# Optimization experiments

Hardware: AMD Instinct MI355X
Metric: run time of the kernel (lower is better)

Reference implementation:

```python
import jax, jax.numpy as jnp
import numpy as np

MASK_FILL = -1e9  # masked_fill_value (avoids NaNs vs -inf)

def setup_inputs() -> dict:
    key = jax.random.key(0)
    k1, k2, k3 = jax.random.split(key, 3)
    B, L, H, E = 4, 2048, 16, 128
    S, D = L, E
    queries = jax.random.normal(k1, (B, L, H, E), dtype=jnp.float32)
    keys = jax.random.normal(k2, (B, S, H, E), dtype=jnp.float32)
    values = jax.random.normal(k3, (B, S, H, D), dtype=jnp.float32)
    return {"queries": queries, "keys": keys, "values": values}

def reference(queries, keys, values):
    B, L, H, E = queries.shape
    S = keys.shape[1]
    scale = 1.0 / jnp.sqrt(jnp.asarray(E, queries.dtype))
    # compute_scores: dot-product scores (B,H,L,S)
    scores = jnp.einsum('blhe,bshe->bhls', queries, keys)
    # causal mask (mask_flag=True, attn_mask=None -> TriangularCausalMask)
    causal = jnp.triu(jnp.ones((L, S), dtype=bool), k=1)  # True above diagonal = masked
    scores = jnp.where(causal[None, None, :, :], MASK_FILL, scores)
    # scale * scores -> softmax (dropout p=0, eval)
    A = jax.nn.softmax(scale * scores, axis=-1)
    # combine_values: (B,H,L,S) x (B,S,H,D) -> (B,L,H,D)
    V = jnp.einsum('bhls,bshd->blhd', A, values)
    return V
```

## Files before the change

kernel.cpp:

```cpp
#include <hip/hip_runtime.h>
#include <hip/hip_bf16.h>

typedef __attribute__((ext_vector_type(4))) float f32x4;
typedef __attribute__((ext_vector_type(2))) float f32x2v;
typedef __attribute__((ext_vector_type(16))) float f32x16;
typedef __attribute__((ext_vector_type(8))) short s16x8;
typedef __attribute__((ext_vector_type(4))) short s16x4;
typedef __attribute__((ext_vector_type(4))) unsigned u32x4v;
typedef __attribute__((ext_vector_type(2))) int i32x2;

static constexpr int Bb = 4, Ll = 2048, Hh = 16, Ee = 128;
static constexpr int RS = Hh * Ee;
static constexpr float SCALE = 0.088388347648318447f;
static constexpr float LOG2E = 1.4426950408889634f;
static constexpr float SCL = SCALE * LOG2E;
static constexpr float MOFF = 26.0f;

__device__ __forceinline__ unsigned pk2bf(float lo, float hi) {
  float2 t = make_float2(lo, hi);
  __hip_bfloat162 b2 = __float22bfloat162_rn(t);
  union { __hip_bfloat162 b; unsigned u; } cv; cv.b = b2;
  return cv.u;
}

__device__ __forceinline__ s16x8 pack8(float a0, float a1, float a2, float a3,
                                       float a4, float a5, float a6, float a7) {
  u32x4v u = { pk2bf(a0,a1), pk2bf(a2,a3), pk2bf(a4,a5), pk2bf(a6,a7) };
  return *(s16x8*)&u;
}

__device__ __forceinline__ void plswap(int &x, int &y, int h5) {
#if __has_builtin(__builtin_amdgcn_permlane32_swap)
  i32x2 r = __builtin_amdgcn_permlane32_swap(x, y, false, false);
  x = r[0]; y = r[1];
#else
  int px = __shfl_xor(x, 32, 64);
  int py = __shfl_xor(y, 32, 64);
  int nx = h5 ? py : x;
  int ny = h5 ? y : px;
  x = nx; y = ny;
#endif
}

__device__ __forceinline__ s16x8 mkpa(float p0, float p1, float p2, float p3,
                                      float p4, float p5, float p6, float p7, int h5) {
  int uA = (int)pk2bf(p0, p1), uB = (int)pk2bf(p2, p3);
  int uC = (int)pk2bf(p4, p5), uD = (int)pk2bf(p6, p7);
  plswap(uA, uC, h5);
  plswap(uB, uD, h5);
  u32x4v u = { (unsigned)uA, (unsigned)uB, (unsigned)uC, (unsigned)uD };
  return *(s16x8*)&u;
}

__device__ __forceinline__ void gl_lds16(const short* g, short* l) {
  __builtin_amdgcn_global_load_lds((const __attribute__((address_space(1))) void*)g,
                                   (__attribute__((address_space(3))) void*)l, 16, 0, 0);
}

__global__ __launch_bounds__(256) void conv_k(const float* __restrict__ src, short* __restrict__ dst) {
  const size_t i = (size_t)blockIdx.x * 256 + threadIdx.x;
  const int c = (int)(i & 15);
  const size_t row = i >> 4;
  const int s = (int)((row >> 4) & 2047);
  const float* p = src + row * 128 + ((c ^ (s & 7)) * 8);
  f32x4 a = *(const f32x4*)p;
  f32x4 b = *(const f32x4*)(p + 4);
  *(s16x8*)(dst + i * 8) = pack8(a[0],a[1],a[2],a[3],b[0],b[1],b[2],b[3]);
}

__global__ __launch_bounds__(256) void conv_vt(const float* __restrict__ V, unsigned* __restrict__ Vt32) {
  const int bh = blockIdx.x >> 4, s0 = (blockIdx.x & 15) * 128;
  const int b = bh >> 4, h = bh & 15;
  const int w = threadIdx.x >> 6, lane = threadIdx.x & 63;
  const float* base = V + ((size_t)(b * Ll + s0 + 32 * w)) * RS + h * Ee + 2 * lane;
  unsigned w0[16], w1[16];
#pragma unroll
  for (int j = 0; j < 16; ++j) {
    f32x2v a = *(const f32x2v*)(base + (size_t)(2 * j) * RS);
    f32x2v c = *(const f32x2v*)(base + (size_t)(2 * j + 1) * RS);
    w0[j] = pk2bf(a[0], c[0]);
    w1[j] = pk2bf(a[1], c[1]);
  }
  const int d0 = 2 * lane, d1 = d0 + 1;
  const int T = (s0 + 32 * w) >> 6;
  const int cbase = 4 * (w & 1);
  unsigned* r0 = Vt32 + ((size_t)(bh * 128 + d0)) * 1024 + T * 32;
  unsigned* r1 = Vt32 + ((size_t)(bh * 128 + d1)) * 1024 + T * 32;
#pragma unroll
  for (int jj = 0; jj < 4; ++jj) {
    *(u32x4v*)(r0 + (((cbase + jj) ^ (d0 & 7)) * 4)) = (u32x4v){w0[4*jj],w0[4*jj+1],w0[4*jj+2],w0[4*jj+3]};
    *(u32x4v*)(r1 + (((cbase + jj) ^ (d1 & 7)) * 4)) = (u32x4v){w1[4*jj],w1[4*jj+1],w1[4*jj+2],w1[4*jj+3]};
  }
}

__global__ __launch_bounds__(256, 2)
void attn_main(const float* __restrict__ Qg, const short* __restrict__ Kws,
               const short* __restrict__ Vtws, float* __restrict__ Og) {
  const int phys = blockIdx.x;
  const int lg = (phys & 7) * 64 + (phys >> 3);
  const int bh = lg >> 3;
  const int q4 = lg & 7;
  const int b = bh >> 4, h = bh & 15;
  const int tid = threadIdx.x, w = tid >> 6, l = tid & 63;
  const int l31 = l & 31, h5 = l >> 5, l7 = l & 7;

  __shared__ __align__(16) short smem[32768];

  const short* srcK[4]; const short* srcV[4];
#pragma unroll
  for (int j = 0; j < 4; ++j) {
    const int rowK = (4 * j + w) * 4 + (l >> 4);
    srcK[j] = Kws + ((size_t)(b * Ll + rowK)) * 2048 + h * 128 + (l & 15) * 8;
    const int dV = (4 * j + w) * 8 + (l >> 3);
    srcV[j] = Vtws + ((size_t)(bh * 128 + dV)) * 2048 + l7 * 8;
  }

#define STAGE(base, kvb) do { \
  _Pragma("unroll") for (int j = 0; j < 4; ++j) \
    gl_lds16(srcK[j] + (size_t)(kvb) * 2048, smem + (base) + (4*j + w) * 512 + l * 8); \
  _Pragma("unroll") for (int j = 0; j < 4; ++j) \
    gl_lds16(srcV[j] + (kvb), smem + (base) + 8192 + (4*j + w) * 512 + l * 8); \
} while (0)

  for (int p = 0; p < 2; ++p) {
    const int qi = p ? (15 - q4) : q4;
    const int qb = qi * 128;

    s16x8 qfrag[8];
    {
      const float* qp = Qg + ((size_t)(b * Ll + qb + 32 * w + l31)) * RS + h * Ee;
#pragma unroll
      for (int ks = 0; ks < 8; ++ks) {
        const int e0 = 16 * ks + 8 * h5;
        f32x4 f0 = *(const f32x4*)(qp + e0);
        f32x4 f1 = *(const f32x4*)(qp + e0 + 4);
        qfrag[ks] = pack8(f0[0]*SCL, f0[1]*SCL, f0[2]*SCL, f0[3]*SCL,
                          f1[0]*SCL, f1[1]*SCL, f1[2]*SCL, f1[3]*SCL);
      }
    }

    f32x16 acc[4];
#pragma unroll
    for (int dt = 0; dt < 4; ++dt)
#pragma unroll
      for (int r = 0; r < 16; ++r) acc[dt][r] = 0.f;
    float lacc = 0.f;

    const int ntiles = 2 * qi + 2;
    const int tmaxw = 2 * qi + (w >> 1);

    STAGE(0, 0);

    for (int t = 0; t < ntiles; ++t) {
      const int cur = t & 1;
      const int cbase = cur ? 16384 : 0;
      if (t + 1 < ntiles) {
        STAGE(cur ? 0 : 16384, 64 * (t + 1));
        asm volatile("s_waitcnt vmcnt(8)" ::: "memory");
      } else {
        asm volatile("s_waitcnt vmcnt(0)" ::: "memory");
      }
      __builtin_amdgcn_s_barrier();
      __builtin_amdgcn_sched_barrier(0);

      if (t <= tmaxw) {
        const short* Kc = smem + cbase;
        const short* Vc = smem + cbase + 8192;
        const bool full2 = (t < tmaxw) || (w & 1);

        f32x16 s0, s1;
#pragma unroll
        for (int r = 0; r < 16; ++r) { s0[r] = 0.f; s1[r] = 0.f; }
        __builtin_amdgcn_s_setprio(1);
#pragma unroll
        for (int ks = 0; ks < 8; ++ks) {
          s16x8 a0 = *(const s16x8*)(Kc + l31 * 128 + (((2 * ks + h5) ^ l7) << 3));
          s0 = __builtin_amdgcn_mfma_f32_32x32x16_bf16(a0, qfrag[ks], s0, 0, 0, 0);
        }
        if (full2) {
#pragma unroll
          for (int ks = 0; ks < 8; ++ks) {
            s16x8 a1 = *(const s16x8*)(Kc + (32 + l31) * 128 + (((2 * ks + h5) ^ l7) << 3));
            s1 = __builtin_amdgcn_mfma_f32_32x32x16_bf16(a1, qfrag[ks], s1, 0, 0, 0);
          }
        }
        __builtin_amdgcn_s_setprio(0);

        if (t == tmaxw) {
          const int qoff = qb + 32 * w - 64 * t + l31;
#pragma unroll
          for (int r = 0; r < 16; ++r) {
            const int kv = (r & 3) + 8 * (r >> 2) + 4 * h5;
            if (kv > qoff) s0[r] = -3.0e38f;
          }
          if (full2) {
#pragma unroll
            for (int r = 0; r < 16; ++r) {
              const int kv = 32 + (r & 3) + 8 * (r >> 2) + 4 * h5;
              if (kv > qoff) s1[r] = -3.0e38f;
            }
          }
        }

        float pv0[16], pv1[16];
#pragma unroll
        for (int r = 0; r < 16; ++r) { const float p2 = exp2f(s0[r] - MOFF); pv0[r] = p2; lacc += p2; }
        if (full2) {
#pragma unroll
          for (int r = 0; r < 16; ++r) { const float p2 = exp2f(s1[r] - MOFF); pv1[r] = p2; lacc += p2; }
        }
        s16x8 pa[4];
        pa[0] = mkpa(pv0[0],pv0[1],pv0[2],pv0[3],pv0[4],pv0[5],pv0[6],pv0[7], h5);
        pa[1] = mkpa(pv0[8],pv0[9],pv0[10],pv0[11],pv0[12],pv0[13],pv0[14],pv0[15], h5);
        if (full2) {
          pa[2] = mkpa(pv1[0],pv1[1],pv1[2],pv1[3],pv1[4],pv1[5],pv1[6],pv1[7], h5);
          pa[3] = mkpa(pv1[8],pv1[9],pv1[10],pv1[11],pv1[12],pv1[13],pv1[14],pv1[15], h5);
        } else {
          pa[2] = pa[0]; pa[3] = pa[1];
        }

        __builtin_amdgcn_s_setprio(1);
#pragma unroll
        for (int dt = 0; dt < 4; ++dt) {
          const int dbase = (32 * dt + l31) * 64;
#pragma unroll
          for (int ks = 0; ks < 4; ++ks) {
            if (ks < 2 || full2) {
              s16x8 av = *(const s16x8*)(Vc + dbase + (((2 * ks + h5) ^ l7) << 3));
              acc[dt] = __builtin_amdgcn_mfma_f32_32x32x16_bf16(av, pa[ks], acc[dt], 0, 0, 0);
            }
          }
        }
        __builtin_amdgcn_s_setprio(0);
      }
      __builtin_amdgcn_sched_barrier(0);
      __builtin_amdgcn_s_barrier();
    }

    float lsum;
    {
      int pb = __builtin_bit_cast(int, lacc), pc = pb;
      plswap(pb, pc, h5);
      lsum = __builtin_bit_cast(float, pb) + __builtin_bit_cast(float, pc);
    }
    const float linv = 1.0f / lsum;

    float* Tp = (float*)smem + w * 4096;
#pragma unroll
    for (int half = 0; half < 2; ++half) {
#pragma unroll
      for (int dt2 = 0; dt2 < 2; ++dt2) {
        const int dt = 2 * half + dt2;
#pragma unroll
        for (int g = 0; g < 4; ++g) {
          f32x4 v = { acc[dt][4*g] * linv, acc[dt][4*g+1] * linv,
                      acc[dt][4*g+2] * linv, acc[dt][4*g+3] * linv };
          *(f32x4*)(Tp + l31 * 68 + dt2 * 32 + g * 8 + h5 * 4) = v;
        }
      }
      asm volatile("s_waitcnt lgkmcnt(0)" ::: "memory");
      __builtin_amdgcn_sched_barrier(0);
#pragma unroll
      for (int pp = 0; pp < 8; ++pp) {
        const int qr = (l >> 4) + 4 * pp;
        f32x4 v = *(const f32x4*)(Tp + qr * 68 + (l & 15) * 4);
        *(f32x4*)(Og + ((size_t)(b * Ll + qb + 32 * w + qr)) * RS + h * Ee + half * 64 + (l & 15) * 4) = v;
      }
      asm volatile("s_waitcnt lgkmcnt(0)" ::: "memory");
      __builtin_amdgcn_sched_barrier(0);
    }

    if (p == 0) __syncthreads();
  }
#undef STAGE
}

static constexpr int VPAD = 66;
__device__ __forceinline__ short f2bf(float f) {
  union { float f; unsigned u; } x; x.f = f;
  unsigned r = x.u + 0x7FFFu + ((x.u >> 16) & 1u);
  return (short)(r >> 16);
}
__global__ __launch_bounds__(256, 4)
void attn_fwd(const float* __restrict__ Qg, const float* __restrict__ Kg,
              const float* __restrict__ Vg, float* __restrict__ Og) {
  const int qi = blockIdx.x;
  const int bh = blockIdx.y;
  const int b = bh >> 4, h = bh & 15;
  const int qb = qi * 64;
  const int tid = threadIdx.x, wave = tid >> 6, lane = tid & 63, lo = lane & 15, hi = lane >> 4;
  __shared__ __align__(16) short Klds[64 * 128];
  __shared__ __align__(16) short Vt[128 * VPAD];
  const float* Qb_ = Qg + (size_t)b * Ll * RS + h * Ee;
  const float* Kb_ = Kg + (size_t)b * Ll * RS + h * Ee;
  const float* Vb_ = Vg + (size_t)b * Ll * RS + h * Ee;
  float* Ob_ = Og + (size_t)b * Ll * RS + h * Ee;
  s16x8 qfrag[4];
  {
    const float* qp = Qb_ + (size_t)(qb + wave * 16 + lo) * RS;
#pragma unroll
    for (int ks = 0; ks < 4; ++ks) {
      const int e0 = 32 * ks + 8 * hi;
      f32x4 f0 = *(const f32x4*)(qp + e0);
      f32x4 f1 = *(const f32x4*)(qp + e0 + 4);
      qfrag[ks] = pack8(f0[0]*SCALE, f0[1]*SCALE, f0[2]*SCALE, f0[3]*SCALE,
                        f1[0]*SCALE, f1[1]*SCALE, f1[2]*SCALE, f1[3]*SCALE);
    }
  }
  f32x4 acc[8];
#pragma unroll
  for (int nt = 0; nt < 8; ++nt) acc[nt] = (f32x4){0.f, 0.f, 0.f, 0.f};
  float mrun = -3.0e38f, lrun = 0.f;
  const int r0 = tid >> 4, c0 = (tid & 15) * 8;
  for (int kvb = 0; kvb <= qb; kvb += 64) {
    __syncthreads();
#pragma unroll
    for (int rr4 = 0; rr4 < 4; ++rr4) {
      const int rr = r0 + 16 * rr4;
      const float* kp = Kb_ + (size_t)(kvb + rr) * RS + c0;
      f32x4 f0 = *(const f32x4*)kp;
      f32x4 f1 = *(const f32x4*)(kp + 4);
      const int off = (rr * 256 + c0 * 2) ^ ((rr & 7) << 4);
      *(s16x8*)((char*)Klds + off) = pack8(f0[0],f0[1],f0[2],f0[3],f1[0],f1[1],f1[2],f1[3]);
    }
#pragma unroll
    for (int kk = 0; kk < 2; ++kk) {
      const int kv0 = (r0 * 2 + kk) * 2;
      const float* vp0 = Vb_ + (size_t)(kvb + kv0) * RS + c0;
      const float* vp1 = vp0 + RS;
      f32x4 a0 = *(const f32x4*)vp0, a1 = *(const f32x4*)(vp0 + 4);
      f32x4 b0 = *(const f32x4*)vp1, b1 = *(const f32x4*)(vp1 + 4);
#pragma unroll
      for (int j = 0; j < 4; ++j)
        *(unsigned*)&Vt[(c0 + j) * VPAD + kv0] = pk2bf(a0[j], b0[j]);
#pragma unroll
      for (int j = 0; j < 4; ++j)
        *(unsigned*)&Vt[(c0 + 4 + j) * VPAD + kv0] = pk2bf(a1[j], b1[j]);
    }
    __syncthreads();
    const bool diag = (kvb == qb);
    f32x4 st[4];
#pragma unroll
    for (int mt = 0; mt < 4; ++mt) {
      f32x4 a4 = (f32x4){0.f, 0.f, 0.f, 0.f};
#pragma unroll
      for (int ks = 0; ks < 4; ++ks) {
        const int row = 16 * mt + lo;
        const int off = (row * 256 + (32 * ks + 8 * hi) * 2) ^ ((row & 7) << 4);
        s16x8 a = *(const s16x8*)((const char*)Klds + off);
        a4 = __builtin_amdgcn_mfma_f32_16x16x32_bf16(a, qfrag[ks], a4, 0, 0, 0);
      }
      st[mt] = a4;
    }
    if (diag) {
      const int qg = 16 * wave + lo;
#pragma unroll
      for (int mt = 0; mt < 4; ++mt)
#pragma unroll
        for (int r = 0; r < 4; ++r)
          if (16 * mt + 4 * hi + r > qg) st[mt][r] = -3.0e38f;
    }
    float mx = -3.0e38f;
#pragma unroll
    for (int mt = 0; mt < 4; ++mt)
#pragma unroll
      for (int r = 0; r < 4; ++r) mx = fmaxf(mx, st[mt][r]);
    mx = fmaxf(mx, __shfl_xor(mx, 16, 64));
    mx = fmaxf(mx, __shfl_xor(mx, 32, 64));
    const float mnew = fmaxf(mrun, mx);
    const float alpha = exp2f((mrun - mnew) * LOG2E);
    float psum = 0.f;
    s16x4 pf[4];
#pragma unroll
    for (int mt = 0; mt < 4; ++mt)
#pragma unroll
      for (int r = 0; r < 4; ++r) {
        const float p = exp2f((st[mt][r] - mnew) * LOG2E);
        psum += p;
        pf[mt][r] = f2bf(p);
      }
    psum += __shfl_xor(psum, 16, 64);
    psum += __shfl_xor(psum, 32, 64);
    lrun = lrun * alpha + psum;
    mrun = mnew;
    float alr[4];
#pragma unroll
    for (int r = 0; r < 4; ++r) alr[r] = __shfl(alpha, 4 * hi + r, 64);
#pragma unroll
    for (int nt = 0; nt < 8; ++nt) {
      acc[nt][0] *= alr[0]; acc[nt][1] *= alr[1];
      acc[nt][2] *= alr[2]; acc[nt][3] *= alr[3];
    }
#pragma unroll
    for (int mt = 0; mt < 4; ++mt)
#pragma unroll
      for (int nt = 0; nt < 8; ++nt) {
        const int hw = (16 * nt + lo) * VPAD + 16 * mt + 4 * hi;
        s16x4 vf = *(const s16x4*)&Vt[hw];
        acc[nt] = __builtin_amdgcn_mfma_f32_16x16x16bf16_1k(pf[mt], vf, acc[nt], 0, 0, 0);
      }
  }
  float linv[4];
#pragma unroll
  for (int r = 0; r < 4; ++r) linv[r] = 1.0f / __shfl(lrun, 4 * hi + r, 64);
#pragma unroll
  for (int r = 0; r < 4; ++r) {
    const int qg = qb + 16 * wave + 4 * hi + r;
    float* op = Ob_ + (size_t)qg * RS + lo;
#pragma unroll
    for (int nt = 0; nt < 8; ++nt)
      op[16 * nt] = acc[nt][r] * linv[r];
  }
}

extern "C" void kernel_launch(void* const* d_in, const int* in_sizes, int n_in,
                              void* d_out, int out_size, void* d_ws, size_t ws_size,
                              hipStream_t stream) {
  const float* Qp = (const float*)d_in[0];
  const float* Kp = (const float*)d_in[1];
  const float* Vp = (const float*)d_in[2];
  float* Op = (float*)d_out;
  const size_t elems = (size_t)Bb * Ll * Hh * Ee;
  if (ws_size >= elems * 2 * 2) {
    short* Kws = (short*)d_ws;
    short* Vtws = Kws + elems;
    conv_k<<<(int)(elems / 8 / 256), 256, 0, stream>>>(Kp, Kws);
    conv_vt<<<Bb * Hh * (Ll / 128), 256, 0, stream>>>(Vp, (unsigned*)Vtws);
    attn_main<<<512, 256, 0, stream>>>(Qp, Kws, Vtws, Op);
  } else {
    dim3 grid(Ll / 64, Bb * Hh);
    attn_fwd<<<grid, 256, 0, stream>>>(Qp, Kp, Vp, Op);
  }
}
```

Measured before the change: 159.2 us.

## Restructure attention into 32-key tiles with padded LDS and one q-block per CTA

Drops the XOR swizzle in the K/V workspace layouts and uses padded LDS rows (272B for K, 80B for V) to avoid bank conflicts instead. The KV tile shrinks from 64 to 32 keys, so each wave does one S tile per step and causal masking is finer. The grid doubles to 1024 blocks, each handling one q-block instead of a light/heavy pair, with occupancy raised to 3 blocks per CU. The output now goes straight to global memory without the LDS transpose. Risks are more barriers per unit of work, less coalesced output stores, and load imbalance across heavy and light q-blocks.

Result: no change. 157.9 us (-0.8%).

```diff
diff --git a/kernel.cpp b/kernel.cpp
--- a/kernel.cpp
+++ b/kernel.cpp
@@ -15,6 +15,12 @@
 static constexpr float LOG2E = 1.4426950408889634f;
 static constexpr float SCL = SCALE * LOG2E;
 static constexpr float MOFF = 26.0f;
+
+static constexpr int KROW = 272;
+static constexpr int KBYTES = 32 * KROW;
+static constexpr int VROW = 80;
+static constexpr int VBYTES = 128 * VROW;
+static constexpr int BUFSZ = KBYTES + VBYTES;
 
 __device__ __forceinline__ unsigned pk2bf(float lo, float hi) {
   float2 t = make_float2(lo, hi);
@@ -58,14 +64,10 @@
 }
 
 __global__ __launch_bounds__(256) void conv_k(const float* __restrict__ src, short* __restrict__ dst) {
-  const size_t i = (size_t)blockIdx.x * 256 + threadIdx.x;
-  const int c = (int)(i & 15);
-  const size_t row = i >> 4;
-  const int s = (int)((row >> 4) & 2047);
-  const float* p = src + row * 128 + ((c ^ (s & 7)) * 8);
-  f32x4 a = *(const f32x4*)p;
-  f32x4 b = *(const f32x4*)(p + 4);
-  *(s16x8*)(dst + i * 8) = pack8(a[0],a[1],a[2],a[3],b[0],b[1],b[2],b[3]);
+  size_t i = ((size_t)blockIdx.x * 256 + threadIdx.x) * 8;
+  f32x4 a = *(const f32x4*)(src + i);
+  f32x4 b = *(const f32x4*)(src + i + 4);
+  *(s16x8*)(dst + i) = pack8(a[0],a[1],a[2],a[3],b[0],b[1],b[2],b[3]);
 }
 
 __global__ __launch_bounds__(256) void conv_vt(const float* __restrict__ V, unsigned* __restrict__ Vt32) {
@@ -81,198 +83,148 @@
     w0[j] = pk2bf(a[0], c[0]);
     w1[j] = pk2bf(a[1], c[1]);
   }
-  const int d0 = 2 * lane, d1 = d0 + 1;
-  const int T = (s0 + 32 * w) >> 6;
-  const int cbase = 4 * (w & 1);
-  unsigned* r0 = Vt32 + ((size_t)(bh * 128 + d0)) * 1024 + T * 32;
-  unsigned* r1 = Vt32 + ((size_t)(bh * 128 + d1)) * 1024 + T * 32;
+  unsigned* r0 = Vt32 + ((size_t)(bh * 128 + 2 * lane)) * 1024 + (s0 + 32 * w) / 2;
+  unsigned* r1 = r0 + 1024;
 #pragma unroll
   for (int jj = 0; jj < 4; ++jj) {
-    *(u32x4v*)(r0 + (((cbase + jj) ^ (d0 & 7)) * 4)) = (u32x4v){w0[4*jj],w0[4*jj+1],w0[4*jj+2],w0[4*jj+3]};
-    *(u32x4v*)(r1 + (((cbase + jj) ^ (d1 & 7)) * 4)) = (u32x4v){w1[4*jj],w1[4*jj+1],w1[4*jj+2],w1[4*jj+3]};
-  }
-}
-
-__global__ __launch_bounds__(256, 2)
+    *(u32x4v*)(r0 + 4 * jj) = (u32x4v){w0[4*jj], w0[4*jj+1], w0[4*jj+2], w0[4*jj+3]};
+    *(u32x4v*)(r1 + 4 * jj) = (u32x4v){w1[4*jj], w1[4*jj+1], w1[4*jj+2], w1[4*jj+3]};
+  }
+}
+
+__global__ __launch_bounds__(256, 3)
 void attn_main(const float* __restrict__ Qg, const short* __restrict__ Kws,
                const short* __restrict__ Vtws, float* __restrict__ Og) {
   const int phys = blockIdx.x;
-  const int lg = (phys & 7) * 64 + (phys >> 3);
-  const int bh = lg >> 3;
-  const int q4 = lg & 7;
+  const int qi = ((phys >> 6) & 1) ? (phys >> 7) : (15 - (phys >> 7));
+  const int bh = phys & 63;
   const int b = bh >> 4, h = bh & 15;
+  const int qb = qi * 128;
   const int tid = threadIdx.x, w = tid >> 6, l = tid & 63;
-  const int l31 = l & 31, h5 = l >> 5, l7 = l & 7;
-
-  __shared__ __align__(16) short smem[32768];
-
-  const short* srcK[4]; const short* srcV[4];
-#pragma unroll
-  for (int j = 0; j < 4; ++j) {
-    const int rowK = (4 * j + w) * 4 + (l >> 4);
-    srcK[j] = Kws + ((size_t)(b * Ll + rowK)) * 2048 + h * 128 + (l & 15) * 8;
-    const int dV = (4 * j + w) * 8 + (l >> 3);
-    srcV[j] = Vtws + ((size_t)(bh * 128 + dV)) * 2048 + l7 * 8;
-  }
-
-#define STAGE(base, kvb) do { \
-  _Pragma("unroll") for (int j = 0; j < 4; ++j) \
-    gl_lds16(srcK[j] + (size_t)(kvb) * 2048, smem + (base) + (4*j + w) * 512 + l * 8); \
-  _Pragma("unroll") for (int j = 0; j < 4; ++j) \
-    gl_lds16(srcV[j] + (kvb), smem + (base) + 8192 + (4*j + w) * 512 + l * 8); \
-} while (0)
-
-  for (int p = 0; p < 2; ++p) {
-    const int qi = p ? (15 - q4) : q4;
-    const int qb = qi * 128;
-
-    s16x8 qfrag[8];
-    {
-      const float* qp = Qg + ((size_t)(b * Ll + qb + 32 * w + l31)) * RS + h * Ee;
+  const int l31 = l & 31, h5 = l >> 5;
+
+  __shared__ __align__(16) short smem[BUFSZ];
+
+  s16x8 qfrag[8];
+  {
+    const float* qp = Qg + ((size_t)(b * Ll + qb + 32 * w + l31)) * RS + h * Ee;
+#pragma unroll
+    for (int ks = 0; ks < 8; ++ks) {
+      const int e0 = 16 * ks + 8 * h5;
+      f32x4 f0 = *(const f32x4*)(qp + e0);
+      f32x4 f1 = *(const f32x4*)(qp + e0 + 4);
+      qfrag[ks] = pack8(f0[0]*SCL, f0[1]*SCL, f0[2]*SCL, f0[3]*SCL,
+                        f1[0]*SCL, f1[1]*SCL, f1[2]*SCL, f1[3]*SCL);
+    }
+  }
+
+  f32x16 acc[4];
+#pragma unroll
+  for (int dt = 0; dt < 4; ++dt)
+#pragma unroll
+    for (int r = 0; r < 16; ++r) acc[dt][r] = 0.f;
+  float lacc = 0.f;
+
+  const short* skp[3]; const short* svp[3];
+  int kdst[3], vdst[3];
+#pragma unroll
+  for (int j = 0; j < 3; ++j) {
+    const int kid = (j < 2) ? (w * 136 + 64 * j + l) : (w * 136 + 128 + (l & 7));
+    const int kr = kid / 17;
+    int ksl = kid % 17; if (ksl == 16) ksl = 0;
+    skp[j] = Kws + ((size_t)(b * Ll + kr)) * 2048 + h * 128 + ksl * 8;
+    kdst[j] = kid * 16;
+    const int vid = (j < 2) ? (w * 160 + 64 * j + l) : (w * 160 + 128 + (l & 31));
+    const int vr = vid / 5;
+    int vsl = vid % 5; if (vsl == 4) vsl = 0;
+    svp[j] = Vtws + ((size_t)(bh * 128 + vr)) * 2048 + vsl * 8;
+    vdst[j] = KBYTES + vid * 16;
+  }
+
+#define STAGE(cb, kvb) do { \
+    gl_lds16(skp[0] + (size_t)(kvb) * 2048, (short*)((char*)smem + (cb) + kdst[0])); \
+    gl_lds16(skp[1] + (size_t)(kvb) * 2048, (short*)((char*)smem + (cb) + kdst[1])); \
+    if (l < 8)  gl_lds16(skp[2] + (size_t)(kvb) * 2048, (short*)((char*)smem + (cb) + kdst[2])); \
+    gl_lds16(svp[0] + (kvb), (short*)((char*)smem + (cb) + vdst[0])); \
+    gl_lds16(svp[1] + (kvb), (short*)((char*)smem + (cb) + vdst[1])); \
+    if (l < 32) gl_lds16(svp[2] + (kvb), (short*)((char*)smem + (cb) + vdst[2])); \
+  } while (0)
+
+  const int ntiles = 4 * qi + 4;
+  const int tmaxw = 4 * qi + w;
+
+  STAGE(0, 0);
+
+  for (int t = 0; t < ntiles; ++t) {
+    const int cbase = (t & 1) ? BUFSZ : 0;
+    if (t + 1 < ntiles) {
+      STAGE(cbase ? 0 : BUFSZ, 32 * (t + 1));
+      asm volatile("s_waitcnt vmcnt(6)" ::: "memory");
+    } else {
+      asm volatile("s_waitcnt vmcnt(0)" ::: "memory");
+    }
+    __builtin_amdgcn_s_barrier();
+    __builtin_amdgcn_sched_barrier(0);
+
+    if (t <= tmaxw) {
+      f32x16 s;
+#pragma unroll
+      for (int r = 0; r < 16; ++r) s[r] = 0.f;
+      __builtin_amdgcn_s_setprio(1);
 #pragma unroll
       for (int ks = 0; ks < 8; ++ks) {
-        const int e0 = 16 * ks + 8 * h5;
-        f32x4 f0 = *(const f32x4*)(qp + e0);
-        f32x4 f1 = *(const f32x4*)(qp + e0 + 4);
-        qfrag[ks] = pack8(f0[0]*SCL, f0[1]*SCL, f0[2]*SCL, f0[3]*SCL,
-                          f1[0]*SCL, f1[1]*SCL, f1[2]*SCL, f1[3]*SCL);
-      }
-    }
-
-    f32x16 acc[4];
-#pragma unroll
-    for (int dt = 0; dt < 4; ++dt)
-#pragma unroll
-      for (int r = 0; r < 16; ++r) acc[dt][r] = 0.f;
-    float lacc = 0.f;
-
-    const int ntiles = 2 * qi + 2;
-    const int tmaxw = 2 * qi + (w >> 1);
-
-    STAGE(0, 0);
-
-    for (int t = 0; t < ntiles; ++t) {
-      const int cur = t & 1;
-      const int cbase = cur ? 16384 : 0;
-      if (t + 1 < ntiles) {
-        STAGE(cur ? 0 : 16384, 64 * (t + 1));
-        asm volatile("s_waitcnt vmcnt(8)" ::: "memory");
-      } else {
-        asm volatile("s_waitcnt vmcnt(0)" ::: "memory");
-      }
-      __builtin_amdgcn_s_barrier();
-      __builtin_amdgcn_sched_barrier(0);
-
-      if (t <= tmaxw) {
-        const short* Kc = smem + cbase;
-        const short* Vc = smem + cbase + 8192;
-        const bool full2 = (t < tmaxw) || (w & 1);
-
-        f32x16 s0, s1;
-#pragma unroll
-        for (int r = 0; r < 16; ++r) { s0[r] = 0.f; s1[r] = 0.f; }
-        __builtin_amdgcn_s_setprio(1);
-#pragma unroll
-        for (int ks = 0; ks < 8; ++ks) {
-          s16x8 a0 = *(const s16x8*)(Kc + l31 * 128 + (((2 * ks + h5) ^ l7) << 3));
-          s0 = __builtin_amdgcn_mfma_f32_32x32x16_bf16(a0, qfrag[ks], s0, 0, 0, 0);
+        s16x8 a = *(const s16x8*)((const char*)smem + cbase + l31 * KROW + h5 * 16 + ks * 32);
+        s = __builtin_amdgcn_mfma_f32_32x32x16_bf16(a, qfrag[ks], s, 0, 0, 0);
+      }
+      __builtin_amdgcn_s_setprio(0);
+
+      if (t == tmaxw) {
+#pragma unroll
+        for (int r = 0; r < 16; ++r) {
+          const int kvl = (r & 3) + 8 * (r >> 2) + 4 * h5;
+          if (kvl > l31) s[r] = -3.0e38f;
         }
-        if (full2) {
-#pragma unroll
-          for (int ks = 0; ks < 8; ++ks) {
-            s16x8 a1 = *(const s16x8*)(Kc + (32 + l31) * 128 + (((2 * ks + h5) ^ l7) << 3));
-            s1 = __builtin_amdgcn_mfma_f32_32x32x16_bf16(a1, qfrag[ks], s1, 0, 0, 0);
-          }
-        }
-        __builtin_amdgcn_s_setprio(0);
-
-        if (t == tmaxw) {
-          const int qoff = qb + 32 * w - 64 * t + l31;
-#pragma unroll
-          for (int r = 0; r < 16; ++r) {
-            const int kv = (r & 3) + 8 * (r >> 2) + 4 * h5;
-            if (kv > qoff) s0[r] = -3.0e38f;
-          }
-          if (full2) {
-#pragma unroll
-            for (int r = 0; r < 16; ++r) {
-              const int kv = 32 + (r & 3) + 8 * (r >> 2) + 4 * h5;
-              if (kv > qoff) s1[r] = -3.0e38f;
-            }
-          }
-        }
-
-        float pv0[16], pv1[16];
-#pragma unroll
-        for (int r = 0; r < 16; ++r) { const float p2 = exp2f(s0[r] - MOFF); pv0[r] = p2; lacc += p2; }
-        if (full2) {
-#pragma unroll
-          for (int r = 0; r < 16; ++r) { const float p2 = exp2f(s1[r] - MOFF); pv1[r] = p2; lacc += p2; }
-        }
-        s16x8 pa[4];
-        pa[0] = mkpa(pv0[0],pv0[1],pv0[2],pv0[3],pv0[4],pv0[5],pv0[6],pv0[7], h5);
-        pa[1] = mkpa(pv0[8],pv0[9],pv0[10],pv0[11],pv0[12],pv0[13],pv0[14],pv0[15], h5);
-        if (full2) {
-          pa[2] = mkpa(pv1[0],pv1[1],pv1[2],pv1[3],pv1[4],pv1[5],pv1[6],pv1[7], h5);
-          pa[3] = mkpa(pv1[8],pv1[9],pv1[10],pv1[11],pv1[12],pv1[13],pv1[14],pv1[15], h5);
-        } else {
-          pa[2] = pa[0]; pa[3] = pa[1];
-        }
-
-        __builtin_amdgcn_s_setprio(1);
-#pragma unroll
-        for (int dt = 0; dt < 4; ++dt) {
-          const int dbase = (32 * dt + l31) * 64;
-#pragma unroll
-          for (int ks = 0; ks < 4; ++ks) {
-            if (ks < 2 || full2) {
-              s16x8 av = *(const s16x8*)(Vc + dbase + (((2 * ks + h5) ^ l7) << 3));
-              acc[dt] = __builtin_amdgcn_mfma_f32_32x32x16_bf16(av, pa[ks], acc[dt], 0, 0, 0);
-            }
-          }
-        }
-        __builtin_amdgcn_s_setprio(0);
-      }
-      __builtin_amdgcn_sched_barrier(0);
-      __builtin_amdgcn_s_barrier();
-    }
-
-    float lsum;
-    {
-      int pb = __builtin_bit_cast(int, lacc), pc = pb;
-      plswap(pb, pc, h5);
-      lsum = __builtin_bit_cast(float, pb) + __builtin_bit_cast(float, pc);
-    }
-    const float linv = 1.0f / lsum;
-
-    float* Tp = (float*)smem + w * 4096;
-#pragma unroll
-    for (int half = 0; half < 2; ++half) {
-#pragma unroll
-      for (int dt2 = 0; dt2 < 2; ++dt2) {
-        const int dt = 2 * half + dt2;
-#pragma unroll
-        for (int g = 0; g < 4; ++g) {
-          f32x4 v = { acc[dt][4*g] * linv, acc[dt][4*g+1] * linv,
-                      acc[dt][4*g+2] * linv, acc[dt][4*g+3] * linv };
-          *(f32x4*)(Tp + l31 * 68 + dt2 * 32 + g * 8 + h5 * 4) = v;
-        }
-      }
-      asm volatile("s_waitcnt lgkmcnt(0)" ::: "memory");
-      __builtin_amdgcn_sched_barrier(0);
-#pragma unroll
-      for (int pp = 0; pp < 8; ++pp) {
-        const int qr = (l >> 4) + 4 * pp;
-        f32x4 v = *(const f32x4*)(Tp + qr * 68 + (l & 15) * 4);
-        *(f32x4*)(Og + ((size_t)(b * Ll + qb + 32 * w + qr)) * RS + h * Ee + half * 64 + (l & 15) * 4) = v;
-      }
-      asm volatile("s_waitcnt lgkmcnt(0)" ::: "memory");
-      __builtin_amdgcn_sched_barrier(0);
-    }
-
-    if (p == 0) __syncthreads();
+      }
+
+      float pv[16];
+#pragma unroll
+      for (int r = 0; r < 16; ++r) { const float p2 = exp2f(s[r] - MOFF); pv[r] = p2; lacc += p2; }
+      s16x8 pa0 = mkpa(pv[0], pv[1], pv[2], pv[3], pv[4], pv[5], pv[6], pv[7], h5);
+      s16x8 pa1 = mkpa(pv[8], pv[9], pv[10], pv[11], pv[12], pv[13], pv[14], pv[15], h5);
+
+      __builtin_amdgcn_s_setprio(1);
+#pragma unroll
+      for (int dt = 0; dt < 4; ++dt) {
+        const int vb = cbase + KBYTES + dt * (32 * VROW) + l31 * VROW + h5 * 16;
+        s16x8 av0 = *(const s16x8*)((const char*)smem + vb);
+        acc[dt] = __builtin_amdgcn_mfma_f32_32x32x16_bf16(av0, pa0, acc[dt], 0, 0, 0);
+        s16x8 av1 = *(const s16x8*)((const char*)smem + vb + 32);
+        acc[dt] = __builtin_amdgcn_mfma_f32_32x32x16_bf16(av1, pa1, acc[dt], 0, 0, 0);
+      }
+      __builtin_amdgcn_s_setprio(0);
+    }
+    __builtin_amdgcn_sched_barrier(0);
+    __builtin_amdgcn_s_barrier();
   }
 #undef STAGE
+
+  float lsum;
+  {
+    int pb = __builtin_bit_cast(int, lacc), pc = pb;
+    plswap(pb, pc, h5);
+    lsum = __builtin_bit_cast(float, pb) + __builtin_bit_cast(float, pc);
+  }
+  const float linv = 1.0f / lsum;
+
+  float* orow = Og + ((size_t)(b * Ll + qb + 32 * w + l31)) * RS + h * Ee;
+#pragma unroll
+  for (int dt = 0; dt < 4; ++dt)
+#pragma unroll
+    for (int g = 0; g < 4; ++g) {
+      f32x4 v = { acc[dt][4*g] * linv, acc[dt][4*g+1] * linv,
+                  acc[dt][4*g+2] * linv, acc[dt][4*g+3] * linv };
+      *(f32x4*)(orow + dt * 32 + g * 8 + h5 * 4) = v;
+    }
 }
 
 static constexpr int VPAD = 66;
@@ -426,7 +378,7 @@
     short* Vtws = Kws + elems;
     conv_k<<<(int)(elems / 8 / 256), 256, 0, stream>>>(Kp, Kws);
     conv_vt<<<Bb * Hh * (Ll / 128), 256, 0, stream>>>(Vp, (unsigned*)Vtws);
-    attn_main<<<512, 256, 0, stream>>>(Qp, Kws, Vtws, Op);
+    attn_main<<<1024, 256, 0, stream>>>(Qp, Kws, Vtws, Op);
   } else {
     dim3 grid(Ll / 64, Bb * Hh);
     attn_fwd<<<grid, 256, 0, stream>>>(Qp, Kp, Vp, Op);
```
